# Kernel tuning notes

Measured on AMD Instinct MI355X. Metric: run time of the kernel, lower is better.

The kernel has to match this reference:

```python
import jax, jax.numpy as jnp
import numpy as np

N = 100000
E = 3200000
D = 64


def setup_inputs() -> dict:
    key = jax.random.key(0)
    k1, k2, k3 = jax.random.split(key, 3)
    indices = jax.random.randint(k1, (2, E), 0, N, dtype=jnp.int64) if jax.config.jax_enable_x64 else jax.random.randint(k1, (2, E), 0, N, dtype=jnp.int32)
    values = jax.random.uniform(k2, (E,), dtype=jnp.float32)
    b = jax.random.normal(k3, (N, D), dtype=jnp.float32)
    return {"indices": indices, "values": values, "shape": N, "b": b}


def reference(indices, values, shape, b):
    # sparse COO [N,N] @ dense [N,D]:
    # out[r] = sum over edges e with row[e]==r of values[e] * b[col[e]]
    row, col = indices[0], indices[1]
    msgs = values[:, None] * b[col]            # [E, D] gather + scale
    out = jax.ops.segment_sum(msgs, row, num_segments=shape)  # [N, D] scatter-add
    return out
```

## Files before the change

kernel.cpp:

```cpp
#include <hip/hip_runtime.h>
#include <hip/hip_bf16.h>


#define D 64
#define BROWS 32
#define MAXNB 4096
#define CAP 1280
#define NM (CAP / 256)
#define SPILLCAP 8192
#define NCHUNK 4
#define NBINS (BROWS * NCHUNK)

#define CROWS 2048
#define NCB 64
#define SCH_A 4096
#define CBLK 4352
#define NBLK_C 16
#define CAPC (CBLK * NBLK_C)

__global__ __launch_bounds__(256) void spmm_atomic_kernel(
    const int* __restrict__ rows, const int* __restrict__ cols,
    const float* __restrict__ vals, const float* __restrict__ b,
    float* __restrict__ out, int E) {
  long long gid = (long long)blockIdx.x * blockDim.x + threadIdx.x;
  int e = (int)(gid >> 6);
  int d = (int)(gid & 63);
  if (e >= E) return;
  atomicAdd(&out[(long long)rows[e] * D + d], vals[e] * b[(long long)cols[e] * D + d]);
}

__device__ __forceinline__ unsigned bf16rne(float x) {
  unsigned u = __float_as_uint(x);
  return (u + 0x7FFFu + ((u >> 16) & 1u)) >> 16;
}
__global__ __launch_bounds__(256) void convert_kernel(
    const float4* __restrict__ src, uint2* __restrict__ dst, int n4) {
  int i = blockIdx.x * 256 + threadIdx.x;
  if (i >= n4) return;
  float4 f = src[i];
  dst[i] = make_uint2(bf16rne(f.x) | (bf16rne(f.y) << 16),
                      bf16rne(f.z) | (bf16rne(f.w) << 16));
}

__global__ __launch_bounds__(256) void coarse_scatter_kernel(
    const int* __restrict__ rows, const int* __restrict__ cols,
    const float* __restrict__ vals, int* __restrict__ gcoarse,
    uint2* __restrict__ cslab_lo, uint2* __restrict__ cslab_hi, int csplit,
    uint4* __restrict__ spill, int* __restrict__ spill_cnt, int E) {
  __shared__ uint2 stage[SCH_A];
  __shared__ unsigned char sbin[SCH_A];
  __shared__ int h[NCB];
  __shared__ int lst[NCB];
  __shared__ int gb[NCB];
  int t = threadIdx.x;
  if (t < NCB) h[t] = 0;
  __syncthreads();
  int start = blockIdx.x * SCH_A;
  int ec = E - start;
  if (ec > SCH_A) ec = SCH_A;
  bool full = (start + SCH_A <= E);

  int4 r4[4];
  int rank[16];
  if (full) {
#pragma unroll
    for (int ki = 0; ki < 4; ki++) {
      r4[ki] = ((const int4*)(rows + start + ki * 1024))[t];
      rank[4 * ki + 0] = atomicAdd(&h[r4[ki].x >> 11], 1);
      rank[4 * ki + 1] = atomicAdd(&h[r4[ki].y >> 11], 1);
      rank[4 * ki + 2] = atomicAdd(&h[r4[ki].z >> 11], 1);
      rank[4 * ki + 3] = atomicAdd(&h[r4[ki].w >> 11], 1);
    }
  } else {
#pragma unroll
    for (int ki = 0; ki < 4; ki++) {
      int e = start + ki * 1024 + t * 4;
      int4 rr = make_int4(-1, -1, -1, -1);
      if (e + 0 < E) { rr.x = rows[e + 0]; rank[4 * ki + 0] = atomicAdd(&h[rr.x >> 11], 1); }
      if (e + 1 < E) { rr.y = rows[e + 1]; rank[4 * ki + 1] = atomicAdd(&h[rr.y >> 11], 1); }
      if (e + 2 < E) { rr.z = rows[e + 2]; rank[4 * ki + 2] = atomicAdd(&h[rr.z >> 11], 1); }
      if (e + 3 < E) { rr.w = rows[e + 3]; rank[4 * ki + 3] = atomicAdd(&h[rr.w >> 11], 1); }
      r4[ki] = rr;
    }
  }
  __syncthreads();
  if (t < NCB) {
    int c = h[t];
    int x = c;
#pragma unroll
    for (int off = 1; off < 64; off <<= 1) {
      int u = __shfl_up(x, off);
      if (t >= off) x += u;
    }
    lst[t] = x - c;
    gb[t] = c ? atomicAdd(&gcoarse[t], c) : 0;
  }
  __syncthreads();
#pragma unroll
  for (int ki = 0; ki < 4; ki++) {
    int e = start + ki * 1024 + t * 4;
    int rr[4] = {r4[ki].x, r4[ki].y, r4[ki].z, r4[ki].w};
    int cc[4];
    float vv[4];
    if (full) {
      int4 c4 = ((const int4*)(cols + start + ki * 1024))[t];
      float4 v4 = ((const float4*)(vals + start + ki * 1024))[t];
      cc[0] = c4.x; cc[1] = c4.y; cc[2] = c4.z; cc[3] = c4.w;
      vv[0] = v4.x; vv[1] = v4.y; vv[2] = v4.z; vv[3] = v4.w;
    } else {
#pragma unroll
      for (int j = 0; j < 4; j++) {
        cc[j] = (e + j < E) ? cols[e + j] : 0;
        vv[j] = (e + j < E) ? vals[e + j] : 0.f;
      }
    }
#pragma unroll
    for (int j = 0; j < 4; j++) {
      if (e + j < E) {
        int r = rr[j];
        int bn = r >> 11;
        int pos = lst[bn] + rank[4 * ki + j];
        stage[pos] = make_uint2(((unsigned)(r & (CROWS - 1)) << 17) |
                                    (unsigned)cc[j],
                                __float_as_uint(vv[j]));
        sbin[pos] = (unsigned char)bn;
      }
    }
  }
  __syncthreads();
  for (int i = t; i < ec; i += 256) {
    int bn = sbin[i];
    uint2 p = stage[i];
    int pin = gb[bn] + (i - lst[bn]);
    if (pin < CAPC) {
      uint2* slab = (bn < csplit) ? (cslab_lo + (size_t)bn * CAPC)
                                  : (cslab_hi + (size_t)(bn - csplit) * CAPC);
      slab[pin] = p;
    } else {
      int sp = atomicAdd(spill_cnt, 1);
      if (sp < SPILLCAP)
        spill[sp] = make_uint4((unsigned)((bn << 11) | (int)(p.x >> 17)),
                               p.x & 0x1FFFFu, p.y, 0u);
    }
  }
}

__global__ __launch_bounds__(256) void fine_scatter_kernel(
    const int* __restrict__ gcoarse, const uint2* __restrict__ cslab_lo,
    const uint2* __restrict__ cslab_hi, int csplit, int* __restrict__ gcount,
    uint2* __restrict__ pairs, uint4* __restrict__ spill,
    int* __restrict__ spill_cnt) {
  int c = blockIdx.x >> 4;
  int blk = blockIdx.x & 15;
  int cnt = gcoarse[c];
  if (cnt > CAPC) cnt = CAPC;
  int base = blk * CBLK;
  int ec = cnt - base;
  if (ec <= 0) return;
  if (ec > CBLK) ec = CBLK;
  const uint2* src = ((c < csplit) ? (cslab_lo + (size_t)c * CAPC)
                                   : (cslab_hi + (size_t)(c - csplit) * CAPC)) +
                     base;
  __shared__ uint2 stage[CBLK];
  __shared__ unsigned char sbin[CBLK];
  __shared__ int h[64];
  __shared__ int lst[64];
  __shared__ int gb[64];
  int t = threadIdx.x;
  if (t < 64) h[t] = 0;
  __syncthreads();
  uint2 mine[17];
  int rank[17];
#pragma unroll
  for (int k = 0; k < 17; k++) {
    int i = k * 256 + t;
    if (i < ec) {
      mine[k] = src[i];
      rank[k] = atomicAdd(&h[(mine[k].x >> 22) & 63u], 1);
    }
  }
  __syncthreads();
  if (t < 64) {
    int cn = h[t];
    int x = cn;
#pragma unroll
    for (int off = 1; off < 64; off <<= 1) {
      int u = __shfl_up(x, off);
      if (t >= off) x += u;
    }
    lst[t] = x - cn;
    gb[t] = cn ? atomicAdd(&gcount[c * 64 + t], cn) : 0;
  }
  __syncthreads();
#pragma unroll
  for (int k = 0; k < 17; k++) {
    int i = k * 256 + t;
    if (i < ec) {
      uint2 p = mine[k];
      int f = (int)((p.x >> 22) & 63u);
      int pos = lst[f] + rank[k];
      unsigned key2 = (((p.x >> 17) & 31u) << 26) | ((p.x & 0x1FFFFu) << 7);
      stage[pos] = make_uint2(key2, p.y);
      sbin[pos] = (unsigned char)f;
    }
  }
  __syncthreads();
  for (int i = t; i < ec; i += 256) {
    int f = sbin[i];
    uint2 p = stage[i];
    int pin = gb[f] + (i - lst[f]);
    int gbkt = c * 64 + f;
    if (pin < CAP) {
      pairs[(size_t)gbkt * CAP + pin] = p;
    } else {
      int sp = atomicAdd(spill_cnt, 1);
      if (sp < SPILLCAP)
        spill[sp] = make_uint4((unsigned)(gbkt * BROWS + (int)(p.x >> 26)),
                               (p.x >> 7) & 0x1FFFFu, p.y, 0u);
    }
  }
}

__global__ __launch_bounds__(256) void spmm_fused_kernel(
    const uint2* __restrict__ pairs, const int* __restrict__ gcount,
    const uint2* __restrict__ b16, float* __restrict__ out, int N) {
  __shared__ uint2 lp[CAP];
  __shared__ int cnt[NBINS];
  __shared__ int roff[NBINS + 1];
  __shared__ int wpart[4];
  int bkt = blockIdx.x;
  int cntE = gcount[bkt];
  if (cntE > CAP) cntE = CAP;
  const uint2* src = pairs + (size_t)bkt * CAP;
  int t = threadIdx.x;
  int lane = t & 63;
  int wv = t >> 6;
  if (t < NBINS) cnt[t] = 0;
  __syncthreads();
  uint2 mine[NM];
  int rk[NM];
#pragma unroll
  for (int k = 0; k < NM; k++) {
    int i = t + k * 256;
    if (i < cntE) {
      mine[k] = src[i];
      int bin = ((mine[k].x >> 26) << 2) | ((mine[k].x >> 22) & 3);
      rk[k] = atomicAdd(&cnt[bin], 1);
    }
  }
  __syncthreads();
  {
    int c0 = (t < NBINS) ? cnt[t] : 0;
    int x = c0;
#pragma unroll
    for (int off = 1; off < 64; off <<= 1) {
      int u = __shfl_up(x, off);
      if (lane >= off) x += u;
    }
    if (lane == 63) wpart[wv] = x;
    __syncthreads();
    if (t < NBINS) {
      int wbase = 0;
      for (int w = 0; w < wv; w++) wbase += wpart[w];
      roff[t] = wbase + x - c0;
      if (t == NBINS - 1) roff[NBINS] = wbase + x;
    }
  }
  __syncthreads();
#pragma unroll
  for (int k = 0; k < NM; k++) {
    int i = t + k * 256;
    if (i < cntE) {
      int bin = ((mine[k].x >> 26) << 2) | ((mine[k].x >> 22) & 3);
      lp[roff[bin] + rk[k]] = make_uint2(mine[k].x & 0x03FFFF80u, mine[k].y);
    }
  }
  __syncthreads();
  int gid = t >> 3;
  int l8 = t & 7;
  const char* bq = (const char*)b16 + (l8 << 4);
  float acc[8] = {0.f, 0.f, 0.f, 0.f, 0.f, 0.f, 0.f, 0.f};
  for (int ch = 0; ch < NCHUNK; ch++) {
    int bin = (gid << 2) | ch;
    int j0 = roff[bin], j1 = roff[bin + 1];
    for (int base = j0; base < j1; base += 4) {
      uint4 bv[4];
      float vv[4];
#pragma unroll
      for (int k = 0; k < 4; k++) {
        int idx = base + k;
        int ic = (idx < j1) ? idx : j0;
        uint2 p = lp[ic];
        bv[k] = *(const uint4*)(bq + p.x);
        vv[k] = (idx < j1) ? __uint_as_float(p.y) : 0.f;
      }
#pragma unroll
      for (int k = 0; k < 4; k++) {
        unsigned u0 = bv[k].x, u1 = bv[k].y, u2 = bv[k].z, u3 = bv[k].w;
        float v = vv[k];
        acc[0] += v * __uint_as_float(u0 << 16);
        acc[1] += v * __uint_as_float(u0 & 0xFFFF0000u);
        acc[2] += v * __uint_as_float(u1 << 16);
        acc[3] += v * __uint_as_float(u1 & 0xFFFF0000u);
        acc[4] += v * __uint_as_float(u2 << 16);
        acc[5] += v * __uint_as_float(u2 & 0xFFFF0000u);
        acc[6] += v * __uint_as_float(u3 << 16);
        acc[7] += v * __uint_as_float(u3 & 0xFFFF0000u);
      }
    }
  }
  int gr = bkt * BROWS + gid;
  if (gr < N) {
    float4* dst = (float4*)(out + (size_t)gr * D + l8 * 8);
    dst[0] = make_float4(acc[0], acc[1], acc[2], acc[3]);
    dst[1] = make_float4(acc[4], acc[5], acc[6], acc[7]);
  }
}

__global__ __launch_bounds__(256) void spill_fix_kernel(
    const uint4* __restrict__ spill, const int* __restrict__ spill_cnt,
    const float* __restrict__ b, float* __restrict__ out) {
  int n = *spill_cnt;
  if (n > SPILLCAP) n = SPILLCAP;
  int lane = threadIdx.x & 63;
  int w = (int)((blockIdx.x * blockDim.x + threadIdx.x) >> 6);
  int nw = (int)((gridDim.x * blockDim.x) >> 6);
  for (int s = w; s < n; s += nw) {
    uint4 e = spill[s];
    atomicAdd(&out[(size_t)e.x * D + lane],
              __uint_as_float(e.z) * b[(size_t)e.y * D + lane]);
  }
}

extern "C" void kernel_launch(void* const* d_in, const int* in_sizes, int n_in,
                              void* d_out, int out_size, void* d_ws, size_t ws_size,
                              hipStream_t stream) {
  const int* indices = (const int*)d_in[0];
  const float* vals  = (const float*)d_in[1];
  const float* b     = (const float*)d_in[3];

  int E = in_sizes[1];
  int N = in_sizes[3] / D;
  const int* rows = indices;
  const int* cols = indices + E;

  int NC = (N + CROWS - 1) / CROWS;
  int n4 = N * D / 4;

  size_t off_gcount  = 0;
  size_t off_gcoarse = off_gcount + (size_t)MAXNB * 4;
  size_t off_scnt    = off_gcoarse + (size_t)NCB * 4;
  size_t off_spill   = (off_scnt + 4 + 15) & ~(size_t)15;
  size_t off_pairs   = off_spill + (size_t)SPILLCAP * 16;
  size_t npbkt       = (size_t)NC * 64;
  size_t off_b16     = off_pairs + npbkt * CAP * 8;
  size_t off_cextra  = off_b16 + (size_t)N * D * 2;
  size_t outbytes    = (size_t)out_size * 4;
  int csplit = (int)(outbytes / ((size_t)CAPC * 8));
  if (csplit > NC) csplit = NC;
  size_t cextra = (size_t)(NC - csplit) * CAPC * 8;
  size_t need2 = off_cextra + cextra;

  if (ws_size >= need2 && NC <= NCB && (int)npbkt <= MAXNB) {
    char*  ws        = (char*)d_ws;
    int*   gcount    = (int*)(ws + off_gcount);
    int*   gcoarse   = (int*)(ws + off_gcoarse);
    int*   spill_cnt = (int*)(ws + off_scnt);
    uint4* spill     = (uint4*)(ws + off_spill);
    uint2* pairs     = (uint2*)(ws + off_pairs);
    uint2* b16       = (uint2*)(ws + off_b16);
    uint2* cslab_lo  = (uint2*)d_out;
    uint2* cslab_hi  = (uint2*)(ws + off_cextra);

    hipMemsetAsync(gcount, 0, (size_t)MAXNB * 4 + (size_t)NCB * 4 + 4, stream);
    convert_kernel<<<(n4 + 255) / 256, 256, 0, stream>>>(
        (const float4*)b, b16, n4);
    coarse_scatter_kernel<<<(E + SCH_A - 1) / SCH_A, 256, 0, stream>>>(
        rows, cols, vals, gcoarse, cslab_lo, cslab_hi, csplit,
        spill, spill_cnt, E);
    fine_scatter_kernel<<<NC * NBLK_C, 256, 0, stream>>>(
        gcoarse, cslab_lo, cslab_hi, csplit, gcount, pairs, spill, spill_cnt);
    spmm_fused_kernel<<<(int)npbkt, 256, 0, stream>>>(pairs, gcount, b16,
                                                      (float*)d_out, N);
    spill_fix_kernel<<<16, 256, 0, stream>>>(spill, spill_cnt, b,
                                             (float*)d_out);
    return;
  }

  hipMemsetAsync(d_out, 0, (size_t)out_size * sizeof(float), stream);
  long long total = (long long)E * 64;
  spmm_atomic_kernel<<<(int)((total + 255) / 256), 256, 0, stream>>>(
      rows, cols, vals, b, (float*)d_out, E);
}
```

Before: 227.0 us.

## Double bucket rows to 64 and pad per-row edge lists to remove tail guards

Fine buckets now cover 64 rows each instead of 32, which halves the number of buckets and fused-kernel blocks and doubles per-bucket capacity and LDS staging. Each row's edge segment is padded to a multiple of 4 with zero-valued entries, so the inner gather loop runs without bounds checks or selects. Each 8-thread group now accumulates two rows, which gives fewer blocks with more work per thread. Larger LDS use may lower occupancy, and the row-bit extraction must match the coarse key encoding.

Measured after the change: 230.5 us. Within noise of the previous version (+1.5%).

```diff
diff --git a/kernel.cpp b/kernel.cpp
--- a/kernel.cpp
+++ b/kernel.cpp
@@ -3,9 +3,10 @@
 
 
 #define D 64
-#define BROWS 32
-#define MAXNB 4096
-#define CAP 1280
+#define BROWS 64
+#define MAXNB 2048
+#define CAP 2560
+#define LPSZ (CAP + 192)
 #define NM (CAP / 256)
 #define SPILLCAP 8192
 #define NCHUNK 4
@@ -163,11 +164,11 @@
                      base;
   __shared__ uint2 stage[CBLK];
   __shared__ unsigned char sbin[CBLK];
-  __shared__ int h[64];
-  __shared__ int lst[64];
-  __shared__ int gb[64];
+  __shared__ int h[32];
+  __shared__ int lst[32];
+  __shared__ int gb[32];
   int t = threadIdx.x;
-  if (t < 64) h[t] = 0;
+  if (t < 32) h[t] = 0;
   __syncthreads();
   uint2 mine[17];
   int rank[17];
@@ -176,20 +177,20 @@
     int i = k * 256 + t;
     if (i < ec) {
       mine[k] = src[i];
-      rank[k] = atomicAdd(&h[(mine[k].x >> 22) & 63u], 1);
-    }
-  }
-  __syncthreads();
-  if (t < 64) {
+      rank[k] = atomicAdd(&h[mine[k].x >> 23], 1);
+    }
+  }
+  __syncthreads();
+  if (t < 32) {
     int cn = h[t];
     int x = cn;
 #pragma unroll
-    for (int off = 1; off < 64; off <<= 1) {
+    for (int off = 1; off < 32; off <<= 1) {
       int u = __shfl_up(x, off);
       if (t >= off) x += u;
     }
     lst[t] = x - cn;
-    gb[t] = cn ? atomicAdd(&gcount[c * 64 + t], cn) : 0;
+    gb[t] = cn ? atomicAdd(&gcount[c * 32 + t], cn) : 0;
   }
   __syncthreads();
 #pragma unroll
@@ -197,9 +198,9 @@
     int i = k * 256 + t;
     if (i < ec) {
       uint2 p = mine[k];
-      int f = (int)((p.x >> 22) & 63u);
+      int f = (int)(p.x >> 23);
       int pos = lst[f] + rank[k];
-      unsigned key2 = (((p.x >> 17) & 31u) << 26) | ((p.x & 0x1FFFFu) << 7);
+      unsigned key2 = (((p.x >> 17) & 63u) << 26) | ((p.x & 0x1FFFFu) << 7);
       stage[pos] = make_uint2(key2, p.y);
       sbin[pos] = (unsigned char)f;
     }
@@ -209,7 +210,7 @@
     int f = sbin[i];
     uint2 p = stage[i];
     int pin = gb[f] + (i - lst[f]);
-    int gbkt = c * 64 + f;
+    int gbkt = c * 32 + f;
     if (pin < CAP) {
       pairs[(size_t)gbkt * CAP + pin] = p;
     } else {
@@ -224,17 +225,15 @@
 __global__ __launch_bounds__(256) void spmm_fused_kernel(
     const uint2* __restrict__ pairs, const int* __restrict__ gcount,
     const uint2* __restrict__ b16, float* __restrict__ out, int N) {
-  __shared__ uint2 lp[CAP];
+  __shared__ uint2 lp[LPSZ];
   __shared__ int cnt[NBINS];
   __shared__ int roff[NBINS + 1];
-  __shared__ int wpart[4];
+  __shared__ int rreal[BROWS];
   int bkt = blockIdx.x;
   int cntE = gcount[bkt];
   if (cntE > CAP) cntE = CAP;
   const uint2* src = pairs + (size_t)bkt * CAP;
   int t = threadIdx.x;
-  int lane = t & 63;
-  int wv = t >> 6;
   if (t < NBINS) cnt[t] = 0;
   __syncthreads();
   uint2 mine[NM];
@@ -249,22 +248,24 @@
     }
   }
   __syncthreads();
-  {
-    int c0 = (t < NBINS) ? cnt[t] : 0;
-    int x = c0;
+  if (t < BROWS) {
+    int c0 = cnt[4 * t + 0], c1 = cnt[4 * t + 1];
+    int c2 = cnt[4 * t + 2], c3 = cnt[4 * t + 3];
+    int s = c0 + c1 + c2 + c3;
+    int pad = (s + 3) & ~3;
+    int x = pad;
 #pragma unroll
     for (int off = 1; off < 64; off <<= 1) {
       int u = __shfl_up(x, off);
-      if (lane >= off) x += u;
-    }
-    if (lane == 63) wpart[wv] = x;
-    __syncthreads();
-    if (t < NBINS) {
-      int wbase = 0;
-      for (int w = 0; w < wv; w++) wbase += wpart[w];
-      roff[t] = wbase + x - c0;
-      if (t == NBINS - 1) roff[NBINS] = wbase + x;
-    }
+      if (t >= off) x += u;
+    }
+    int base = x - pad;
+    roff[4 * t + 0] = base;
+    roff[4 * t + 1] = base + c0;
+    roff[4 * t + 2] = base + c0 + c1;
+    roff[4 * t + 3] = base + c0 + c1 + c2;
+    rreal[t] = base + s;
+    if (t == BROWS - 1) roff[NBINS] = x;
   }
   __syncthreads();
 #pragma unroll
@@ -275,45 +276,59 @@
       lp[roff[bin] + rk[k]] = make_uint2(mine[k].x & 0x03FFFF80u, mine[k].y);
     }
   }
-  __syncthreads();
-  int gid = t >> 3;
-  int l8 = t & 7;
+  if (t < BROWS) {
+    int e0 = rreal[t], e1 = roff[4 * t + 4];
+    for (int i = e0; i < e1; i++) lp[i] = make_uint2(0u, 0u);
+  }
+  __syncthreads();
+  int lane = t & 63;
+  int wv = t >> 6;
+  int g = lane >> 3;
+  int l8 = lane & 7;
+  int gid32 = wv * 8 + g;
   const char* bq = (const char*)b16 + (l8 << 4);
-  float acc[8] = {0.f, 0.f, 0.f, 0.f, 0.f, 0.f, 0.f, 0.f};
-  for (int ch = 0; ch < NCHUNK; ch++) {
-    int bin = (gid << 2) | ch;
-    int j0 = roff[bin], j1 = roff[bin + 1];
+  int row_base = bkt * BROWS;
+  float2 acc[2][4];
+#pragma unroll
+  for (int rr = 0; rr < 2; rr++)
+#pragma unroll
+    for (int j = 0; j < 4; j++) acc[rr][j] = make_float2(0.f, 0.f);
+#pragma unroll
+  for (int rr = 0; rr < 2; rr++) {
+    int r = gid32 + 32 * rr;
+    int j0 = roff[r << 2], j1 = roff[(r << 2) + 4];
     for (int base = j0; base < j1; base += 4) {
       uint4 bv[4];
       float vv[4];
 #pragma unroll
       for (int k = 0; k < 4; k++) {
-        int idx = base + k;
-        int ic = (idx < j1) ? idx : j0;
-        uint2 p = lp[ic];
+        uint2 p = lp[base + k];
         bv[k] = *(const uint4*)(bq + p.x);
-        vv[k] = (idx < j1) ? __uint_as_float(p.y) : 0.f;
+        vv[k] = __uint_as_float(p.y);
       }
 #pragma unroll
       for (int k = 0; k < 4; k++) {
         unsigned u0 = bv[k].x, u1 = bv[k].y, u2 = bv[k].z, u3 = bv[k].w;
         float v = vv[k];
-        acc[0] += v * __uint_as_float(u0 << 16);
-        acc[1] += v * __uint_as_float(u0 & 0xFFFF0000u);
-        acc[2] += v * __uint_as_float(u1 << 16);
-        acc[3] += v * __uint_as_float(u1 & 0xFFFF0000u);
-        acc[4] += v * __uint_as_float(u2 << 16);
-        acc[5] += v * __uint_as_float(u2 & 0xFFFF0000u);
-        acc[6] += v * __uint_as_float(u3 << 16);
-        acc[7] += v * __uint_as_float(u3 & 0xFFFF0000u);
+        acc[rr][0].x += v * __uint_as_float(u0 << 16);
+        acc[rr][0].y += v * __uint_as_float(u0 & 0xFFFF0000u);
+        acc[rr][1].x += v * __uint_as_float(u1 << 16);
+        acc[rr][1].y += v * __uint_as_float(u1 & 0xFFFF0000u);
+        acc[rr][2].x += v * __uint_as_float(u2 << 16);
+        acc[rr][2].y += v * __uint_as_float(u2 & 0xFFFF0000u);
+        acc[rr][3].x += v * __uint_as_float(u3 << 16);
+        acc[rr][3].y += v * __uint_as_float(u3 & 0xFFFF0000u);
       }
     }
   }
-  int gr = bkt * BROWS + gid;
-  if (gr < N) {
-    float4* dst = (float4*)(out + (size_t)gr * D + l8 * 8);
-    dst[0] = make_float4(acc[0], acc[1], acc[2], acc[3]);
-    dst[1] = make_float4(acc[4], acc[5], acc[6], acc[7]);
+#pragma unroll
+  for (int rr = 0; rr < 2; rr++) {
+    int gr = row_base + gid32 + 32 * rr;
+    if (gr < N) {
+      float4* dst = (float4*)(out + (size_t)gr * D + l8 * 8);
+      dst[0] = make_float4(acc[rr][0].x, acc[rr][0].y, acc[rr][1].x, acc[rr][1].y);
+      dst[1] = make_float4(acc[rr][2].x, acc[rr][2].y, acc[rr][3].x, acc[rr][3].y);
+    }
   }
 }
 
@@ -352,7 +367,7 @@
   size_t off_scnt    = off_gcoarse + (size_t)NCB * 4;
   size_t off_spill   = (off_scnt + 4 + 15) & ~(size_t)15;
   size_t off_pairs   = off_spill + (size_t)SPILLCAP * 16;
-  size_t npbkt       = (size_t)NC * 64;
+  size_t npbkt       = (size_t)NC * 32;
   size_t off_b16     = off_pairs + npbkt * CAP * 8;
   size_t off_cextra  = off_b16 + (size_t)N * D * 2;
   size_t outbytes    = (size_t)out_size * 4;
```
